# Kernel optimization log

Hardware: AMD Instinct MI355X
Metric: run time of the kernel (lower is better)

## Reference

```python
import jax, jax.numpy as jnp
import numpy as np

B, N, E = 2, 50000, 400000
FIN, HID, OUT = 128, 128, 128
EPS = 1e-5  # BatchNorm1d default eps


def setup_inputs() -> dict:
    key = jax.random.key(0)
    ks = jax.random.split(key, 12)
    x = jax.random.normal(ks[0], (B, N, FIN), dtype=jnp.float32)
    row = jax.random.randint(ks[1], (E,), 0, N, dtype=jnp.int32)          # scatter dst
    col = jnp.concatenate([jnp.arange(N, dtype=jnp.int32),                # ensure deg>=1
                           jax.random.randint(ks[2], (E - N,), 0, N, dtype=jnp.int32)])
    edge_index = jnp.stack([row, col])                                    # [2, E]
    deg = jnp.zeros((N,), jnp.float32).at[col].add(1.0)                   # degree(col, N)
    dis = deg ** -0.5
    norm = (dis[row] * dis[col])[None, :, None]                           # [1, E, 1]
    W1 = jax.random.normal(ks[3], (HID, FIN), jnp.float32) / np.sqrt(FIN)
    b1 = jax.random.normal(ks[4], (HID,), jnp.float32) * 0.01
    g1 = jnp.ones((N,), jnp.float32)
    be1 = jnp.zeros((N,), jnp.float32)
    W2 = jax.random.normal(ks[5], (OUT, HID), jnp.float32) / np.sqrt(HID)
    b2 = jax.random.normal(ks[6], (OUT,), jnp.float32) * 0.01
    g2 = jnp.ones((N,), jnp.float32)
    be2 = jnp.zeros((N,), jnp.float32)
    return {"x": x, "edge_index": edge_index, "norm": norm,
            "W1": W1, "b1": b1, "g1": g1, "be1": be1,
            "W2": W2, "b2": b2, "g2": g2, "be2": be2}


def _gcn_layer(x, edge_index, norm, W, b, g, be):
    # Linear (dropout p=0 -> identity)
    h = jnp.einsum('bnf,of->bno', x, W) + b                 # [B, N, C]
    # BatchNorm1d(num_features=N): per-node stats over (batch, channel)
    mu = jnp.mean(h, axis=(0, 2), keepdims=True)            # [1, N, 1]
    var = jnp.var(h, axis=(0, 2), keepdims=True)            # biased, as torch
    y = g[None, :, None] * (h - mu) * jax.lax.rsqrt(var + EPS) + be[None, :, None]
    a = jax.nn.gelu(y, approximate=False)                   # torch GELU = exact erf
    # message passing: gather src nodes, scale by norm, scatter-add to dst
    msgs = a[:, edge_index[1], :] * norm                    # [B, E, C]
    return jnp.zeros_like(a).at[:, edge_index[0], :].add(msgs)


def reference(x, edge_index, norm, W1, b1, g1, be1, W2, b2, g2, be2):
    x = _gcn_layer(x, edge_index, norm, W1, b1, g1, be1)
    x = _gcn_layer(x, edge_index, norm, W2, b2, g2, be2)
    return x
```

## Files before the change

### kernel.cpp

```cpp
#include <hip/hip_runtime.h>
#include <math.h>

#define CC 128

typedef unsigned short u16;
typedef short bf16x8 __attribute__((ext_vector_type(8)));
typedef float f32x4 __attribute__((ext_vector_type(4)));

typedef __attribute__((address_space(3))) void lds_t;
typedef const __attribute__((address_space(1))) void gbl_t;

__device__ __forceinline__ u16 f2bf(float f) {
    union { float f; unsigned u; } v; v.f = f;
    unsigned u = v.u;
    return (u16)((u + 0x7FFFu + ((u >> 16) & 1u)) >> 16);
}
__device__ __forceinline__ float bf2f(unsigned hi16) {
    union { unsigned u; float f; } v; v.u = hi16 << 16; return v.f;
}
__device__ __forceinline__ unsigned cvt_pk(float lo, float hi) {
    unsigned r;
    asm("v_cvt_pk_bf16_f32 %0, %1, %2" : "=v"(r) : "v"(lo), "v"(hi));
    return r;
}

__device__ __forceinline__ float gelu_f(float y) {
    float xa = fabsf(y) * 0.70710678118654752f;
    float t  = __builtin_amdgcn_rcpf(fmaf(0.3275911f, xa, 1.0f));
    float p  = fmaf(1.061405429f, t, -1.453152027f);
    p = fmaf(p, t, 1.421413741f);
    p = fmaf(p, t, -0.284496736f);
    p = fmaf(p, t, 0.254829592f);
    p *= t;
    float e  = __expf(-xa * xa);
    float er = fmaf(-p, e, 1.0f);
    float s  = copysignf(er, y);
    return 0.5f * y * (1.0f + s);
}


__global__ __launch_bounds__(256) void k_hist(const int* __restrict__ row, int* __restrict__ cnt, int E) {
    int e = blockIdx.x * 256 + threadIdx.x;
    if (e < E) atomicAdd(&cnt[row[e]], 1);
}

__device__ __forceinline__ int wave_incl_scan(int v) {
    #pragma unroll
    for (int d = 1; d < 64; d <<= 1) {
        int t = __shfl_up(v, d);
        if ((threadIdx.x & 63) >= d) v += t;
    }
    return v;
}

__global__ __launch_bounds__(256) void k_scan_a(const int* __restrict__ cnt, int* __restrict__ bsum, int N) {
    int base = blockIdx.x * 1024 + threadIdx.x * 4;
    int s = 0;
    #pragma unroll
    for (int u = 0; u < 4; ++u) { int i = base + u; if (i < N) s += cnt[i]; }
    #pragma unroll
    for (int d = 32; d > 0; d >>= 1) s += __shfl_down(s, d);
    __shared__ int wsum[4];
    if ((threadIdx.x & 63) == 0) wsum[threadIdx.x >> 6] = s;
    __syncthreads();
    if (threadIdx.x == 0) bsum[blockIdx.x] = wsum[0] + wsum[1] + wsum[2] + wsum[3];
}

__global__ __launch_bounds__(64) void k_scan_b(const int* __restrict__ bsum, int* __restrict__ boff,
                                               int* __restrict__ off, int N, int nb) {
    int carry = 0;
    for (int base = 0; base < nb; base += 64) {
        int t = base + (int)threadIdx.x;
        int v = (t < nb) ? bsum[t] : 0;
        int incl = wave_incl_scan(v);
        if (t < nb) boff[t] = carry + incl - v;
        carry += __shfl(incl, 63);
    }
    if (threadIdx.x == 0) off[N] = carry;
}

__global__ __launch_bounds__(256) void k_scan_c(int* __restrict__ cnt, const int* __restrict__ boff,
                                                int* __restrict__ off, int N) {
    int t = threadIdx.x;
    int base = blockIdx.x * 1024 + t * 4;
    int v[4]; int s = 0;
    #pragma unroll
    for (int u = 0; u < 4; ++u) { int i = base + u; v[u] = (i < N) ? cnt[i] : 0; s += v[u]; }
    int incl = wave_incl_scan(s);
    __shared__ int wsum[4];
    int w = t >> 6, lane = t & 63;
    if (lane == 63) wsum[w] = incl;
    __syncthreads();
    int run = incl - s + boff[blockIdx.x];
    for (int ww = 0; ww < w; ++ww) run += wsum[ww];
    #pragma unroll
    for (int u = 0; u < 4; ++u) {
        int i = base + u;
        if (i < N) { off[i] = run; cnt[i] = 0; }
        run += v[u];
    }
}

__global__ __launch_bounds__(256) void k_fill(const int* __restrict__ row, const int* __restrict__ col,
                                              const float* __restrict__ nrm, const int* __restrict__ off,
                                              int* __restrict__ cur, int2* __restrict__ eg, int E) {
    int e = blockIdx.x * 256 + threadIdx.x;
    if (e < E) {
        int r = row[e];
        int p = off[r] + atomicAdd(&cur[r], 1);
        eg[p] = make_int2(col[e], __float_as_int(nrm[e]));
    }
}

__global__ __launch_bounds__(256) void k_prep(int* __restrict__ cur, int N,
                                              const float* __restrict__ W1, u16* __restrict__ Wp1,
                                              const float* __restrict__ W2, u16* __restrict__ Wp2) {
    int i = blockIdx.x * 256 + threadIdx.x;
    if (i < N) { cur[i] = 0; return; }
    int iw = i - N;
    if (iw < 2 * CC * CC) {
        int is2 = (iw >= CC * CC);
        int ii = is2 ? iw - CC * CC : iw;
        int j = ii & 7, l = (ii >> 3) & 63, s = (ii >> 9) & 3, t = ii >> 11;
        int r = 16 * t + (l & 15);
        int p = s * 32 + ((l >> 4) & 3) * 8 + j;
        if (is2) {
            int k = (p & 7) * 16 + (p >> 3);
            Wp2[ii] = f2bf(W2[r * CC + k]);
        } else {
            Wp1[ii] = f2bf(W1[r * CC + p]);
        }
    }
}

__global__ __launch_bounds__(256, 2) void k_fused_l1(
    const float* __restrict__ X, const u16* __restrict__ Wp1, const u16* __restrict__ Wp2,
    const float* __restrict__ bias, const float* __restrict__ gamma, const float* __restrict__ beta,
    u16* __restrict__ Z, int N)
{
    __shared__ __align__(16) u16 WS1[CC * CC];
    __shared__ __align__(16) u16 WS2[CC * CC];
    __shared__ __align__(16) unsigned TT[4][16][64];

    const int tid = threadIdx.x;
    const int w = tid >> 6;
    const int l = tid & 63;
    const int g = l >> 4;
    const int c = l & 15;
    const int ntiles = (N + 31) / 32;
    const int NB = gridDim.x;

    #pragma unroll
    for (int it = 0; it < 8; ++it) {
        const u16* g1s = Wp1 + it * 2048 + w * 512 + l * 8;
        const u16* g2s = Wp2 + it * 2048 + w * 512 + l * 8;
        __builtin_amdgcn_global_load_lds((gbl_t*)g1s, (lds_t*)&WS1[it * 2048 + w * 512], 16, 0, 0);
        __builtin_amdgcn_global_load_lds((gbl_t*)g2s, (lds_t*)&WS2[it * 2048 + w * 512], 16, 0, 0);
    }

    float bb[8];
    #pragma unroll
    for (int t = 0; t < 8; ++t) bb[t] = bias[t * 16 + c];

    float4 xlo[4], xhi[4];
    float gamv[4], betv[4];
    auto prefetch = [&](int tt) {
        int n8 = tt * 32 + w * 8;
        int nb_ = (n8 < N) ? n8 : 0;
        const float* xb = X + ((size_t)(c >> 3) * N + nb_ + (c & 7)) * CC + g * 8;
        #pragma unroll
        for (int s = 0; s < 4; ++s) {
            xlo[s] = *(const float4*)(xb + s * 32);
            xhi[s] = *(const float4*)(xb + s * 32 + 4);
        }
        #pragma unroll
        for (int r = 0; r < 4; ++r) {
            int p = (4 * g + r) & 7;
            gamv[r] = gamma[nb_ + p];
            betv[r] = beta[nb_ + p];
        }
    };
    prefetch(blockIdx.x);

    __syncthreads();

    for (int t = blockIdx.x; t < ntiles; t += NB) {
        const int n8 = t * 32 + w * 8;
        const bool valid = n8 < N;

        bf16x8 af[4];
        #pragma unroll
        for (int s = 0; s < 4; ++s) {
            unsigned aw[4];
            aw[0] = cvt_pk(xlo[s].x, xlo[s].y); aw[1] = cvt_pk(xlo[s].z, xlo[s].w);
            aw[2] = cvt_pk(xhi[s].x, xhi[s].y); aw[3] = cvt_pk(xhi[s].z, xhi[s].w);
            af[s] = *(bf16x8*)aw;
        }
        float gam[4], bet[4];
        #pragma unroll
        for (int r = 0; r < 4; ++r) { gam[r] = gamv[r]; bet[r] = betv[r]; }

        if (t + NB < ntiles) prefetch(t + NB);

        f32x4 acc[8];
        #pragma unroll
        for (int q = 0; q < 8; ++q) acc[q] = (f32x4){0.f, 0.f, 0.f, 0.f};
        #pragma unroll
        for (int s = 0; s < 4; ++s) {
            bf16x8 bf[8];
            #pragma unroll
            for (int q = 0; q < 8; ++q)
                bf[q] = *(const bf16x8*)&WS1[((q * 4 + s) * 64 + l) * 8];
            #pragma unroll
            for (int q = 0; q < 8; ++q)
                acc[q] = __builtin_amdgcn_mfma_f32_16x16x32_bf16(af[s], bf[q], acc[q], 0, 0, 0);
        }

        float rs[4] = {0.f, 0.f, 0.f, 0.f}, rq[4] = {0.f, 0.f, 0.f, 0.f};
        #pragma unroll
        for (int q = 0; q < 8; ++q)
            #pragma unroll
            for (int r = 0; r < 4; ++r) {
                float h = acc[q][r] + bb[q];
                acc[q][r] = h;
                rs[r] += h;
                rq[r] += h * h;
            }
        #pragma unroll
        for (int d = 1; d < 16; d <<= 1) {
            #pragma unroll
            for (int r = 0; r < 4; ++r) {
                rs[r] += __shfl_xor(rs[r], d);
                rq[r] += __shfl_xor(rq[r], d);
            }
        }
        #pragma unroll
        for (int r = 0; r < 4; ++r) {
            rs[r] += __shfl_xor(rs[r], 32);
            rq[r] += __shfl_xor(rq[r], 32);
        }

        #pragma unroll
        for (int r = 0; r < 4; ++r) {
            float mean = rs[r] * (1.f / 256.f);
            float var  = rq[r] * (1.f / 256.f) - mean * mean;
            float sc = gam[r] * rsqrtf(fmaxf(var, 0.f) + 1e-5f);
            float sh = bet[r] - mean * sc;
            #pragma unroll
            for (int q = 0; q < 8; ++q)
                acc[q][r] = gelu_f(acc[q][r] * sc + sh);
        }

        #pragma unroll
        for (int r = 0; r < 4; ++r) {
            int row = 4 * g + r;
            unsigned tw[4];
            #pragma unroll
            for (int tt = 0; tt < 4; ++tt)
                tw[tt] = cvt_pk(acc[2 * tt][r], acc[2 * tt + 1][r]);
            int colw = (c * 4) ^ ((row & 7) << 2);
            *(uint4*)&TT[w][row][colw] = *(uint4*)tw;
        }
        bf16x8 af2[4];
        #pragma unroll
        for (int s = 0; s < 4; ++s) {
            int colr = (s * 16 + g * 4) ^ ((c & 7) << 2);
            af2[s] = *(const bf16x8*)&TT[w][c][colr];
        }

        f32x4 acc2[8];
        #pragma unroll
        for (int q = 0; q < 8; ++q) acc2[q] = (f32x4){0.f, 0.f, 0.f, 0.f};
        #pragma unroll
        for (int s = 0; s < 4; ++s) {
            bf16x8 bf[8];
            #pragma unroll
            for (int q = 0; q < 8; ++q)
                bf[q] = *(const bf16x8*)&WS2[((q * 4 + s) * 64 + l) * 8];
            #pragma unroll
            for (int q = 0; q < 8; ++q)
                acc2[q] = __builtin_amdgcn_mfma_f32_16x16x32_bf16(af2[s], bf[q], acc2[q], 0, 0, 0);
        }

        if (valid) {
            #pragma unroll
            for (int r = 0; r < 4; ++r) {
                int rr = 4 * g + r;
                int db = rr >> 3, dn = n8 + (rr & 7);
                unsigned zw[4];
                #pragma unroll
                for (int tt = 0; tt < 4; ++tt)
                    zw[tt] = cvt_pk(acc2[2 * tt][r], acc2[2 * tt + 1][r]);
                *(uint4*)(Z + ((size_t)dn * 2 + db) * CC + c * 8) = *(uint4*)zw;
            }
        }
    }
}

__global__ __launch_bounds__(256) void k_agg_bn(
    const u16* __restrict__ Zin, const int* __restrict__ off, const int2* __restrict__ eg,
    const float* __restrict__ b2, const float* __restrict__ g2, const float* __restrict__ be2,
    u16* __restrict__ A2, int N)
{
    __shared__ u16 TW[4][2][256];
    const int wv = threadIdx.x >> 6;
    const int l = threadIdx.x & 63;
    const int half = l >> 5;
    const int h = l & 31;
    const int b = h >> 4;
    const int c = h & 15;
    const int n = blockIdx.x * 8 + wv * 2 + half;
    const bool nv = n < N;
    const int nn = nv ? n : 0;
    const u16* Ab = Zin + b * CC + c * 8;

    float bb[8];
    #pragma unroll
    for (int t = 0; t < 8; ++t) bb[t] = b2[t * 16 + c];

    int s = off[nn];
    int e = nv ? off[nn + 1] : 0;
    float a[8] = {0.f, 0.f, 0.f, 0.f, 0.f, 0.f, 0.f, 0.f};
    for (int j = s; j < e; j += 4) {
        int2 e0 = eg[j], e1 = eg[j + 1], e2 = eg[j + 2], e3 = eg[j + 3];
        int s0 = e0.x;                  float w0 = __int_as_float(e0.y);
        int s1 = (j + 1 < e) ? e1.x : 0; float w1 = (j + 1 < e) ? __int_as_float(e1.y) : 0.f;
        int s2 = (j + 2 < e) ? e2.x : 0; float w2 = (j + 2 < e) ? __int_as_float(e2.y) : 0.f;
        int s3 = (j + 3 < e) ? e3.x : 0; float w3 = (j + 3 < e) ? __int_as_float(e3.y) : 0.f;
        bf16x8 v0 = *(const bf16x8*)(Ab + (size_t)s0 * 256);
        bf16x8 v1 = *(const bf16x8*)(Ab + (size_t)s1 * 256);
        bf16x8 v2 = *(const bf16x8*)(Ab + (size_t)s2 * 256);
        bf16x8 v3 = *(const bf16x8*)(Ab + (size_t)s3 * 256);
        #pragma unroll
        for (int q = 0; q < 8; ++q) {
            a[q] = fmaf(w0, bf2f((u16)v0[q]), a[q]);
            a[q] = fmaf(w1, bf2f((u16)v1[q]), a[q]);
            a[q] = fmaf(w2, bf2f((u16)v2[q]), a[q]);
            a[q] = fmaf(w3, bf2f((u16)v3[q]), a[q]);
        }
    }

    float ss = 0.f, qq = 0.f;
    #pragma unroll
    for (int t = 0; t < 8; ++t) {
        float hh = a[t] + bb[t];
        a[t] = hh;
        ss += hh;
        qq += hh * hh;
    }
    #pragma unroll
    for (int d = 1; d < 32; d <<= 1) {
        ss += __shfl_xor(ss, d);
        qq += __shfl_xor(qq, d);
    }
    float mean = ss * (1.f / 256.f);
    float var  = qq * (1.f / 256.f) - mean * mean;
    float sc = g2[nn] * rsqrtf(fmaxf(var, 0.f) + 1e-5f);
    float sh = be2[nn] - mean * sc;

    #pragma unroll
    for (int t = 0; t < 8; ++t)
        TW[wv][half][b * CC + t * 16 + c] = f2bf(gelu_f(a[t] * sc + sh));
    if (nv) {
        bf16x8 v = *(const bf16x8*)&TW[wv][half][h * 8];
        *(bf16x8*)(A2 + (size_t)nn * 256 + h * 8) = v;
    }
}

__global__ __launch_bounds__(256) void k_agg_out(
    const u16* __restrict__ A2, const int* __restrict__ off, const int2* __restrict__ eg,
    float* __restrict__ Out, int N)
{
    const int wv = threadIdx.x >> 6;
    const int l = threadIdx.x & 63;
    const int half = l >> 5;
    const int h = l & 31;
    const int b = h >> 4;
    const int c = h & 15;
    const int n = blockIdx.x * 8 + wv * 2 + half;
    const bool nv = n < N;
    const int nn = nv ? n : 0;
    const u16* Ab = A2 + h * 8;

    int s = off[nn];
    int e = nv ? off[nn + 1] : 0;
    float a[8] = {0.f, 0.f, 0.f, 0.f, 0.f, 0.f, 0.f, 0.f};
    for (int j = s; j < e; j += 4) {
        int2 e0 = eg[j], e1 = eg[j + 1], e2 = eg[j + 2], e3 = eg[j + 3];
        int s0 = e0.x;                  float w0 = __int_as_float(e0.y);
        int s1 = (j + 1 < e) ? e1.x : 0; float w1 = (j + 1 < e) ? __int_as_float(e1.y) : 0.f;
        int s2 = (j + 2 < e) ? e2.x : 0; float w2 = (j + 2 < e) ? __int_as_float(e2.y) : 0.f;
        int s3 = (j + 3 < e) ? e3.x : 0; float w3 = (j + 3 < e) ? __int_as_float(e3.y) : 0.f;
        bf16x8 v0 = *(const bf16x8*)(Ab + (size_t)s0 * 256);
        bf16x8 v1 = *(const bf16x8*)(Ab + (size_t)s1 * 256);
        bf16x8 v2 = *(const bf16x8*)(Ab + (size_t)s2 * 256);
        bf16x8 v3 = *(const bf16x8*)(Ab + (size_t)s3 * 256);
        #pragma unroll
        for (int q = 0; q < 8; ++q) {
            a[q] = fmaf(w0, bf2f((u16)v0[q]), a[q]);
            a[q] = fmaf(w1, bf2f((u16)v1[q]), a[q]);
            a[q] = fmaf(w2, bf2f((u16)v2[q]), a[q]);
            a[q] = fmaf(w3, bf2f((u16)v3[q]), a[q]);
        }
    }
    if (nv) {
        float* d = Out + ((size_t)b * N + nn) * CC + c * 8;
        *(float4*)&d[0] = make_float4(a[0], a[1], a[2], a[3]);
        *(float4*)&d[4] = make_float4(a[4], a[5], a[6], a[7]);
    }
}


extern "C" void kernel_launch(void* const* d_in, const int* in_sizes, int n_in,
                              void* d_out, int out_size, void* d_ws, size_t ws_size,
                              hipStream_t stream)
{
    const float* x   = (const float*)d_in[0];
    const int*   ei  = (const int*)d_in[1];
    const float* nrm = (const float*)d_in[2];
    const float* W1  = (const float*)d_in[3];
    const float* b1  = (const float*)d_in[4];
    const float* g1  = (const float*)d_in[5];
    const float* be1 = (const float*)d_in[6];
    const float* W2  = (const float*)d_in[7];
    const float* b2  = (const float*)d_in[8];
    const float* g2  = (const float*)d_in[9];
    const float* be2 = (const float*)d_in[10];

    const int N = in_sizes[5];
    const int E = in_sizes[2];
    const int* row = ei;
    const int* col = ei + E;
    const int nb = (N + 1023) / 1024;

    auto al = [](size_t v) { return (v + 255) & ~(size_t)255; };
    char* p = (char*)d_ws;
    int* off    = (int*)p;   p += al((size_t)(N + 1) * 4);
    int* cur    = (int*)p;   p += al((size_t)N * 4);
    int2* eg    = (int2*)p;  p += al((size_t)(E + 8) * 8);
    int* bsum   = (int*)p;   p += al((size_t)nb * 4);
    int* boff   = (int*)p;   p += al((size_t)nb * 4);
    u16* Wp1    = (u16*)p;   p += al((size_t)CC * CC * 2);
    u16* Wp2    = (u16*)p;   p += al((size_t)CC * CC * 2);
    u16* Zbuf   = (u16*)p;   p += al((size_t)2 * N * CC * 2);
    u16* A2buf  = (u16*)p;   p += al((size_t)2 * N * CC * 2);

    const int prep_n = N + 2 * CC * CC;
    k_prep<<<(prep_n + 255) / 256, 256, 0, stream>>>(cur, N, W1, Wp1, W2, Wp2);
    k_hist<<<(E + 255) / 256, 256, 0, stream>>>(row, cur, E);
    k_scan_a<<<nb, 256, 0, stream>>>(cur, bsum, N);
    k_scan_b<<<1, 64, 0, stream>>>(bsum, boff, off, N, nb);
    k_scan_c<<<nb, 256, 0, stream>>>(cur, boff, off, N);
    k_fill<<<(E + 255) / 256, 256, 0, stream>>>(row, col, nrm, off, cur, eg, E);

    const int ga = (N + 7) / 8;
    k_fused_l1<<<512, 256, 0, stream>>>(x, Wp1, Wp2, b1, g1, be1, Zbuf, N);
    k_agg_bn<<<ga, 256, 0, stream>>>(Zbuf, off, eg, b2, g2, be2, A2buf, N);
    k_agg_out<<<ga, 256, 0, stream>>>(A2buf, off, eg, (float*)d_out, N);
}
```

Before: 150.2 us.

## Split gather-aggregation into channel chunks with chunk-major feature layout

Stores intermediate features in a chunk-major layout (8 chunks of 32 channels, each laid out node-contiguous). Aggregation kernels now run one block per slice and chunk, with 4 lanes spread over edges and shuffle reductions across them. The aim is a smaller per-chunk working set (about 3.2 MB each) that stays in cache during random gathers. Because the BN statistics of layer 2 need all chunks, that step is split into a partial-stats pass plus a separate normalize+GELU kernel. This adds an extra kernel, an extra bf16 intermediate buffer and stats traffic, and re-reads the edge list once per chunk.

After: 184.9 us. +23.1%, slower.

```diff
diff --git a/kernel.cpp b/kernel.cpp
--- a/kernel.cpp
+++ b/kernel.cpp
@@ -114,7 +114,8 @@
 
 __global__ __launch_bounds__(256) void k_prep(int* __restrict__ cur, int N,
                                               const float* __restrict__ W1, u16* __restrict__ Wp1,
-                                              const float* __restrict__ W2, u16* __restrict__ Wp2) {
+                                              const float* __restrict__ W2, u16* __restrict__ Wp2,
+                                              const float* __restrict__ b2, float* __restrict__ b2p) {
     int i = blockIdx.x * 256 + threadIdx.x;
     if (i < N) { cur[i] = 0; return; }
     int iw = i - N;
@@ -130,13 +131,16 @@
         } else {
             Wp1[ii] = f2bf(W1[r * CC + p]);
         }
-    }
+        return;
+    }
+    int ip = iw - 2 * CC * CC;
+    if (ip < CC) b2p[ip] = b2[(ip & 7) * 16 + (ip >> 3)];
 }
 
 __global__ __launch_bounds__(256, 2) void k_fused_l1(
     const float* __restrict__ X, const u16* __restrict__ Wp1, const u16* __restrict__ Wp2,
     const float* __restrict__ bias, const float* __restrict__ gamma, const float* __restrict__ beta,
-    u16* __restrict__ Z, int N)
+    u16* __restrict__ Zc, int N)
 {
     __shared__ __align__(16) u16 WS1[CC * CC];
     __shared__ __align__(16) u16 WS2[CC * CC];
@@ -291,120 +295,149 @@
                 #pragma unroll
                 for (int tt = 0; tt < 4; ++tt)
                     zw[tt] = cvt_pk(acc2[2 * tt][r], acc2[2 * tt + 1][r]);
-                *(uint4*)(Z + ((size_t)dn * 2 + db) * CC + c * 8) = *(uint4*)zw;
+                size_t chunk = (size_t)(db * 4 + (c >> 2));
+                *(uint4*)(Zc + (chunk * N + dn) * 32 + (c & 3) * 8) = *(uint4*)zw;
             }
         }
     }
 }
 
-__global__ __launch_bounds__(256) void k_agg_bn(
-    const u16* __restrict__ Zin, const int* __restrict__ off, const int2* __restrict__ eg,
-    const float* __restrict__ b2, const float* __restrict__ g2, const float* __restrict__ be2,
-    u16* __restrict__ A2, int N)
+__global__ __launch_bounds__(256) void k_agg_chunk(
+    const u16* __restrict__ Zc, const int* __restrict__ off, const int2* __restrict__ eg,
+    const float* __restrict__ b2p, u16* __restrict__ H, float2* __restrict__ stats, int N)
 {
-    __shared__ u16 TW[4][2][256];
+    const int cid = blockIdx.x & 7;
+    const int slice = blockIdx.x >> 3;
     const int wv = threadIdx.x >> 6;
     const int l = threadIdx.x & 63;
-    const int half = l >> 5;
-    const int h = l & 31;
-    const int b = h >> 4;
-    const int c = h & 15;
-    const int n = blockIdx.x * 8 + wv * 2 + half;
+    const int ng = l >> 4;
+    const int w16 = l & 15;
+    const int es = w16 >> 2;
+    const int q = w16 & 3;
+    const int n = slice * 16 + wv * 4 + ng;
     const bool nv = n < N;
     const int nn = nv ? n : 0;
-    const u16* Ab = Zin + b * CC + c * 8;
-
-    float bb[8];
-    #pragma unroll
-    for (int t = 0; t < 8; ++t) bb[t] = b2[t * 16 + c];
+    const u16* Zb = Zc + ((size_t)cid * N) * 32 + q * 8;
 
     int s = off[nn];
     int e = nv ? off[nn + 1] : 0;
     float a[8] = {0.f, 0.f, 0.f, 0.f, 0.f, 0.f, 0.f, 0.f};
     for (int j = s; j < e; j += 4) {
-        int2 e0 = eg[j], e1 = eg[j + 1], e2 = eg[j + 2], e3 = eg[j + 3];
-        int s0 = e0.x;                  float w0 = __int_as_float(e0.y);
-        int s1 = (j + 1 < e) ? e1.x : 0; float w1 = (j + 1 < e) ? __int_as_float(e1.y) : 0.f;
-        int s2 = (j + 2 < e) ? e2.x : 0; float w2 = (j + 2 < e) ? __int_as_float(e2.y) : 0.f;
-        int s3 = (j + 3 < e) ? e3.x : 0; float w3 = (j + 3 < e) ? __int_as_float(e3.y) : 0.f;
-        bf16x8 v0 = *(const bf16x8*)(Ab + (size_t)s0 * 256);
-        bf16x8 v1 = *(const bf16x8*)(Ab + (size_t)s1 * 256);
-        bf16x8 v2 = *(const bf16x8*)(Ab + (size_t)s2 * 256);
-        bf16x8 v3 = *(const bf16x8*)(Ab + (size_t)s3 * 256);
-        #pragma unroll
-        for (int q = 0; q < 8; ++q) {
-            a[q] = fmaf(w0, bf2f((u16)v0[q]), a[q]);
-            a[q] = fmaf(w1, bf2f((u16)v1[q]), a[q]);
-            a[q] = fmaf(w2, bf2f((u16)v2[q]), a[q]);
-            a[q] = fmaf(w3, bf2f((u16)v3[q]), a[q]);
-        }
-    }
-
+        int idx = j + es;
+        int2 ed = eg[idx];
+        bool ok = idx < e;
+        int   src = ok ? ed.x : 0;
+        float wt  = ok ? __int_as_float(ed.y) : 0.f;
+        bf16x8 v = *(const bf16x8*)(Zb + (size_t)src * 32);
+        #pragma unroll
+        for (int i = 0; i < 8; ++i)
+            a[i] = fmaf(wt, bf2f((u16)v[i]), a[i]);
+    }
+    #pragma unroll
+    for (int i = 0; i < 8; ++i) {
+        a[i] += __shfl_xor(a[i], 4);
+        a[i] += __shfl_xor(a[i], 8);
+    }
     float ss = 0.f, qq = 0.f;
     #pragma unroll
-    for (int t = 0; t < 8; ++t) {
-        float hh = a[t] + bb[t];
-        a[t] = hh;
-        ss += hh;
-        qq += hh * hh;
-    }
-    #pragma unroll
-    for (int d = 1; d < 32; d <<= 1) {
-        ss += __shfl_xor(ss, d);
-        qq += __shfl_xor(qq, d);
-    }
+    for (int i = 0; i < 8; ++i) {
+        float h = a[i] + b2p[(cid & 3) * 32 + q * 8 + i];
+        a[i] = h;
+        ss += h;
+        qq += h * h;
+    }
+    ss += __shfl_xor(ss, 1); ss += __shfl_xor(ss, 2);
+    qq += __shfl_xor(qq, 1); qq += __shfl_xor(qq, 2);
+
+    if (nv && es == 0) {
+        unsigned hw[4];
+        #pragma unroll
+        for (int tt = 0; tt < 4; ++tt)
+            hw[tt] = cvt_pk(a[2 * tt], a[2 * tt + 1]);
+        *(uint4*)(H + ((size_t)cid * N + nn) * 32 + q * 8) = *(uint4*)hw;
+        if (q == 0) stats[(size_t)cid * N + nn] = make_float2(ss, qq);
+    }
+}
+
+__global__ __launch_bounds__(256) void k_bn2(
+    const u16* __restrict__ H, const float2* __restrict__ stats,
+    const float* __restrict__ g2, const float* __restrict__ be2,
+    u16* __restrict__ A2s, int N)
+{
+    __shared__ u16 TR[4][2][256];
+    const int wv = threadIdx.x >> 6;
+    const int l = threadIdx.x & 63;
+    const int half = l >> 5;
+    const int hl = l & 31;
+    const int n = blockIdx.x * 8 + wv * 2 + half;
+    const bool nv = n < N;
+    const int nn = nv ? n : 0;
+
+    float ss = 0.f, qq = 0.f;
+    if (hl < 8) {
+        float2 st = stats[(size_t)hl * N + nn];
+        ss = st.x; qq = st.y;
+    }
+    ss += __shfl_xor(ss, 1); ss += __shfl_xor(ss, 2); ss += __shfl_xor(ss, 4);
+    qq += __shfl_xor(qq, 1); qq += __shfl_xor(qq, 2); qq += __shfl_xor(qq, 4);
+    ss = __shfl(ss, half * 32);
+    qq = __shfl(qq, half * 32);
     float mean = ss * (1.f / 256.f);
     float var  = qq * (1.f / 256.f) - mean * mean;
     float sc = g2[nn] * rsqrtf(fmaxf(var, 0.f) + 1e-5f);
     float sh = be2[nn] - mean * sc;
 
-    #pragma unroll
-    for (int t = 0; t < 8; ++t)
-        TW[wv][half][b * CC + t * 16 + c] = f2bf(gelu_f(a[t] * sc + sh));
-    if (nv) {
-        bf16x8 v = *(const bf16x8*)&TW[wv][half][h * 8];
-        *(bf16x8*)(A2 + (size_t)nn * 256 + h * 8) = v;
-    }
-}
-
-__global__ __launch_bounds__(256) void k_agg_out(
-    const u16* __restrict__ A2, const int* __restrict__ off, const int2* __restrict__ eg,
+    const int chunk = hl >> 2;
+    const int db = chunk >> 2;
+    bf16x8 hv = *(const bf16x8*)(H + ((size_t)chunk * N + nn) * 32 + (hl & 3) * 8);
+    #pragma unroll
+    for (int i = 0; i < 8; ++i) {
+        float y = bf2f((u16)hv[i]) * sc + sh;
+        TR[wv][half][db * CC + i * 16 + (hl & 15)] = f2bf(gelu_f(y));
+    }
+    bf16x8 ov = *(const bf16x8*)&TR[wv][half][hl * 8];
+    if (nv)
+        *(bf16x8*)(A2s + ((size_t)(hl >> 2) * N + nn) * 32 + (hl & 3) * 8) = ov;
+}
+
+__global__ __launch_bounds__(256) void k_agg_out_chunk(
+    const u16* __restrict__ A2s, const int* __restrict__ off, const int2* __restrict__ eg,
     float* __restrict__ Out, int N)
 {
+    const int cid = blockIdx.x & 7;
+    const int slice = blockIdx.x >> 3;
     const int wv = threadIdx.x >> 6;
     const int l = threadIdx.x & 63;
-    const int half = l >> 5;
-    const int h = l & 31;
-    const int b = h >> 4;
-    const int c = h & 15;
-    const int n = blockIdx.x * 8 + wv * 2 + half;
+    const int ng = l >> 4;
+    const int w16 = l & 15;
+    const int es = w16 >> 2;
+    const int q = w16 & 3;
+    const int n = slice * 16 + wv * 4 + ng;
     const bool nv = n < N;
     const int nn = nv ? n : 0;
-    const u16* Ab = A2 + h * 8;
+    const u16* Ab = A2s + ((size_t)cid * N) * 32 + q * 8;
 
     int s = off[nn];
     int e = nv ? off[nn + 1] : 0;
     float a[8] = {0.f, 0.f, 0.f, 0.f, 0.f, 0.f, 0.f, 0.f};
     for (int j = s; j < e; j += 4) {
-        int2 e0 = eg[j], e1 = eg[j + 1], e2 = eg[j + 2], e3 = eg[j + 3];
-        int s0 = e0.x;                  float w0 = __int_as_float(e0.y);
-        int s1 = (j + 1 < e) ? e1.x : 0; float w1 = (j + 1 < e) ? __int_as_float(e1.y) : 0.f;
-        int s2 = (j + 2 < e) ? e2.x : 0; float w2 = (j + 2 < e) ? __int_as_float(e2.y) : 0.f;
-        int s3 = (j + 3 < e) ? e3.x : 0; float w3 = (j + 3 < e) ? __int_as_float(e3.y) : 0.f;
-        bf16x8 v0 = *(const bf16x8*)(Ab + (size_t)s0 * 256);
-        bf16x8 v1 = *(const bf16x8*)(Ab + (size_t)s1 * 256);
-        bf16x8 v2 = *(const bf16x8*)(Ab + (size_t)s2 * 256);
-        bf16x8 v3 = *(const bf16x8*)(Ab + (size_t)s3 * 256);
-        #pragma unroll
-        for (int q = 0; q < 8; ++q) {
-            a[q] = fmaf(w0, bf2f((u16)v0[q]), a[q]);
-            a[q] = fmaf(w1, bf2f((u16)v1[q]), a[q]);
-            a[q] = fmaf(w2, bf2f((u16)v2[q]), a[q]);
-            a[q] = fmaf(w3, bf2f((u16)v3[q]), a[q]);
-        }
-    }
-    if (nv) {
-        float* d = Out + ((size_t)b * N + nn) * CC + c * 8;
+        int idx = j + es;
+        int2 ed = eg[idx];
+        bool ok = idx < e;
+        int   src = ok ? ed.x : 0;
+        float wt  = ok ? __int_as_float(ed.y) : 0.f;
+        bf16x8 v = *(const bf16x8*)(Ab + (size_t)src * 32);
+        #pragma unroll
+        for (int i = 0; i < 8; ++i)
+            a[i] = fmaf(wt, bf2f((u16)v[i]), a[i]);
+    }
+    #pragma unroll
+    for (int i = 0; i < 8; ++i) {
+        a[i] += __shfl_xor(a[i], 4);
+        a[i] += __shfl_xor(a[i], 8);
+    }
+    if (nv && es == 0) {
+        float* d = Out + ((size_t)(cid >> 2) * N + nn) * CC + (cid & 3) * 32 + q * 8;
         *(float4*)&d[0] = make_float4(a[0], a[1], a[2], a[3]);
         *(float4*)&d[4] = make_float4(a[4], a[5], a[6], a[7]);
     }
@@ -435,26 +468,31 @@
 
     auto al = [](size_t v) { return (v + 255) & ~(size_t)255; };
     char* p = (char*)d_ws;
-    int* off    = (int*)p;   p += al((size_t)(N + 1) * 4);
-    int* cur    = (int*)p;   p += al((size_t)N * 4);
-    int2* eg    = (int2*)p;  p += al((size_t)(E + 8) * 8);
-    int* bsum   = (int*)p;   p += al((size_t)nb * 4);
-    int* boff   = (int*)p;   p += al((size_t)nb * 4);
-    u16* Wp1    = (u16*)p;   p += al((size_t)CC * CC * 2);
-    u16* Wp2    = (u16*)p;   p += al((size_t)CC * CC * 2);
-    u16* Zbuf   = (u16*)p;   p += al((size_t)2 * N * CC * 2);
-    u16* A2buf  = (u16*)p;   p += al((size_t)2 * N * CC * 2);
-
-    const int prep_n = N + 2 * CC * CC;
-    k_prep<<<(prep_n + 255) / 256, 256, 0, stream>>>(cur, N, W1, Wp1, W2, Wp2);
+    int* off     = (int*)p;    p += al((size_t)(N + 1) * 4);
+    int* cur     = (int*)p;    p += al((size_t)N * 4);
+    int2* eg     = (int2*)p;   p += al((size_t)(E + 8) * 8);
+    int* bsum    = (int*)p;    p += al((size_t)nb * 4);
+    int* boff    = (int*)p;    p += al((size_t)nb * 4);
+    u16* Wp1     = (u16*)p;    p += al((size_t)CC * CC * 2);
+    u16* Wp2     = (u16*)p;    p += al((size_t)CC * CC * 2);
+    float* b2p   = (float*)p;  p += al((size_t)CC * 4);
+    u16* Zc      = (u16*)p;    p += al((size_t)2 * N * CC * 2);
+    u16* Hbuf    = (u16*)p;    p += al((size_t)2 * N * CC * 2);
+    u16* A2s     = (u16*)p;    p += al((size_t)2 * N * CC * 2);
+    float2* stat = (float2*)p; p += al((size_t)8 * N * 8);
+
+    const int prep_n = N + 2 * CC * CC + CC;
+    k_prep<<<(prep_n + 255) / 256, 256, 0, stream>>>(cur, N, W1, Wp1, W2, Wp2, b2, b2p);
     k_hist<<<(E + 255) / 256, 256, 0, stream>>>(row, cur, E);
     k_scan_a<<<nb, 256, 0, stream>>>(cur, bsum, N);
     k_scan_b<<<1, 64, 0, stream>>>(bsum, boff, off, N, nb);
     k_scan_c<<<nb, 256, 0, stream>>>(cur, boff, off, N);
     k_fill<<<(E + 255) / 256, 256, 0, stream>>>(row, col, nrm, off, cur, eg, E);
 
-    const int ga = (N + 7) / 8;
-    k_fused_l1<<<512, 256, 0, stream>>>(x, Wp1, Wp2, b1, g1, be1, Zbuf, N);
-    k_agg_bn<<<ga, 256, 0, stream>>>(Zbuf, off, eg, b2, g2, be2, A2buf, N);
-    k_agg_out<<<ga, 256, 0, stream>>>(A2buf, off, eg, (float*)d_out, N);
-}
+    k_fused_l1<<<512, 256, 0, stream>>>(x, Wp1, Wp2, b1, g1, be1, Zc, N);
+
+    const int nslice = (N + 15) / 16;
+    k_agg_chunk<<<nslice * 8, 256, 0, stream>>>(Zc, off, eg, b2p, Hbuf, stat, N);
+    k_bn2<<<(N + 7) / 8, 256, 0, stream>>>(Hbuf, stat, g2, be2, A2s, N);
+    k_agg_out_chunk<<<nslice * 8, 256, 0, stream>>>(A2s, off, eg, (float*)d_out, N);
+}
```
